# Kernel tuning notes

Measured on AMD Instinct MI355X. Metric: run time of the kernel, lower is better.

The kernel has to match this reference:

```python
import jax, jax.numpy as jnp
import numpy as np

KERNEL_SIZE = 11
OUT_CH = 512
IN_CH = 512


def make_pos_grid(k):
    # centered integer offsets, grid flattened at the end: shape (2, k*k)
    coords = jnp.arange(k, dtype=jnp.float32) - (k - 1) / 2.0
    yy, xx = jnp.meshgrid(coords, coords, indexing="ij")
    return jnp.stack([yy.reshape(-1), xx.reshape(-1)], axis=0)  # (2, k*k)


def setup_inputs() -> dict:
    key = jax.random.key(0)
    k1, _ = jax.random.split(key)
    # raw Cholesky parameters per (out_channel, in_channel) pair; diagonal goes
    # through exp() in reference() to guarantee positive-definite covariances.
    chol_raw = 0.1 * jax.random.normal(k1, (OUT_CH, IN_CH, 2, 2), dtype=jnp.float32)
    pos_grid = make_pos_grid(KERNEL_SIZE)
    return {"chol_raw": chol_raw, "pos_grid": pos_grid}


def reference(chol_raw, pos_grid):
    # chol_raw: (O, I, 2, 2) raw params; pos_grid: (2, K) with K = k*k
    O, I = chol_raw.shape[0], chol_raw.shape[1]
    K = pos_grid.shape[-1]
    k = int(round(np.sqrt(K)))

    # Lower-triangular Cholesky factor with positive diagonal:
    # L = [[exp(a), 0], [c, exp(d)]]
    l11 = jnp.exp(chol_raw[..., 0, 0])[..., None]  # (O, I, 1)
    l21 = chol_raw[..., 1, 0][..., None]           # (O, I, 1)
    l22 = jnp.exp(chol_raw[..., 1, 1])[..., None]  # (O, I, 1)

    x1 = pos_grid[0]  # (K,)
    x2 = pos_grid[1]  # (K,)

    # Inlined forward substitution: solve L b = x for each (o, i, position)
    b1 = x1 / l11                    # (O, I, K)
    b2 = (x2 - l21 * b1) / l22       # (O, I, K)

    # dists = sum over the 2-vector of squares = x^T S^{-1} x
    dists = (b1 * b1 + b2 * b2).reshape((O, I, k, k))
    return dists
```

## Files before the change

kernel.cpp:

```cpp
#include <hip/hip_runtime.h>

#define KK 121
#define NPAIR (512 * 512)
#define PPB 64
#define NBLK (NPAIR / PPB)
#define STAGE_F4 (PPB * KK / 4)

__global__ __launch_bounds__(256) void
quad_rank3_kernel(const float4* __restrict__ chol4,
                  const float* __restrict__ pg,
                  float4* __restrict__ out4) {
    __shared__ float4 s_uvw[KK];
    __shared__ __align__(16) float stage[PPB * KK];

    const int t = threadIdx.x;

    if (t < KK) {
        float x1 = pg[t];
        float x2 = pg[KK + t];
        float4 g;
        g.x = x1 * x1; g.y = x2 * x2; g.z = x1 * x2; g.w = 0.f;
        s_uvw[t] = g;
    }

    const int p       = t & 63;
    const int quarter = t >> 6;
    const int k0 = (quarter == 0) ? 0 : (30 * quarter + 1);
    const int k1 = (quarter == 0) ? 31 : (k0 + 30);

    float4 c = chol4[blockIdx.x * PPB + p];
    float e1 = __expf(-c.x);
    float e2 = __expf(-c.w);
    float f  = c.z * e2;
    float P  = e1 * e1 * fmaf(f, f, 1.f);
    float Q  = e2 * e2;
    float R  = -2.f * f * e1 * e2;

    __syncthreads();

    float* st = &stage[p * KK];
#pragma unroll 5
    for (int k = k0; k < k1; ++k) {
        float4 g = s_uvw[k];
        st[k] = fmaf(P, g.x, fmaf(Q, g.y, R * g.z));
    }

    __syncthreads();

    const float4* s4 = (const float4*)stage;
    float4* o = out4 + (size_t)blockIdx.x * STAGE_F4;
#pragma unroll
    for (int i = t; i < STAGE_F4; i += 256) {
        o[i] = s4[i];
    }
}

extern "C" void kernel_launch(void* const* d_in, const int* in_sizes, int n_in,
                              void* d_out, int out_size, void* d_ws, size_t ws_size,
                              hipStream_t stream) {
    const float4* chol4 = (const float4*)d_in[0];
    const float* pg     = (const float*)d_in[1];
    float4* out4        = (float4*)d_out;

    quad_rank3_kernel<<<NBLK, 256, 0, stream>>>(chol4, pg, out4);
}
```

Baseline: 131.3 us.

## Compute outputs directly per float4 and stream with nontemporal stores, dropping LDS staging

Removes the 31KB shared-memory staging buffer and the second barrier. Each thread now computes four consecutive output elements straight from per-pair coefficients and grid terms held in shared memory, using a multiply-shift division by 121, and writes them with nontemporal float4 stores. Launch bounds now request 8 blocks per CU. The aim is higher occupancy and less LDS traffic in a write-bound kernel, at the cost of extra index arithmetic and scattered LDS reads per element.

```diff
diff --git a/kernel.cpp b/kernel.cpp
--- a/kernel.cpp
+++ b/kernel.cpp
@@ -4,54 +4,51 @@
 #define NPAIR (512 * 512)
 #define PPB 64
 #define NBLK (NPAIR / PPB)
-#define STAGE_F4 (PPB * KK / 4)
+#define F4PB (PPB * KK / 4)
 
-__global__ __launch_bounds__(256) void
-quad_rank3_kernel(const float4* __restrict__ chol4,
-                  const float* __restrict__ pg,
-                  float4* __restrict__ out4) {
+typedef float floatx4 __attribute__((ext_vector_type(4)));
+
+__global__ __launch_bounds__(256, 8) void
+quad_stream_kernel(const float4* __restrict__ chol4,
+                   const float* __restrict__ pg,
+                   float4* __restrict__ out4) {
+    __shared__ float4 s_pqr[PPB];
     __shared__ float4 s_uvw[KK];
-    __shared__ __align__(16) float stage[PPB * KK];
 
     const int t = threadIdx.x;
 
     if (t < KK) {
         float x1 = pg[t];
         float x2 = pg[KK + t];
-        float4 g;
-        g.x = x1 * x1; g.y = x2 * x2; g.z = x1 * x2; g.w = 0.f;
-        s_uvw[t] = g;
+        s_uvw[t] = make_float4(x1 * x1, x2 * x2, x1 * x2, 0.f);
     }
-
-    const int p       = t & 63;
-    const int quarter = t >> 6;
-    const int k0 = (quarter == 0) ? 0 : (30 * quarter + 1);
-    const int k1 = (quarter == 0) ? 31 : (k0 + 30);
-
-    float4 c = chol4[blockIdx.x * PPB + p];
-    float e1 = __expf(-c.x);
-    float e2 = __expf(-c.w);
-    float f  = c.z * e2;
-    float P  = e1 * e1 * fmaf(f, f, 1.f);
-    float Q  = e2 * e2;
-    float R  = -2.f * f * e1 * e2;
-
+    if (t < PPB) {
+        float4 c = chol4[blockIdx.x * PPB + t];
+        float e1 = __expf(-c.x);
+        float e2 = __expf(-c.w);
+        float f  = c.z * e2;
+        float P  = e1 * e1 * fmaf(f, f, 1.f);
+        float Q  = e2 * e2;
+        float R  = -2.f * f * e1 * e2;
+        s_pqr[t] = make_float4(P, Q, R, 0.f);
+    }
     __syncthreads();
 
-    float* st = &stage[p * KK];
-#pragma unroll 5
-    for (int k = k0; k < k1; ++k) {
-        float4 g = s_uvw[k];
-        st[k] = fmaf(P, g.x, fmaf(Q, g.y, R * g.z));
-    }
-
-    __syncthreads();
-
-    const float4* s4 = (const float4*)stage;
-    float4* o = out4 + (size_t)blockIdx.x * STAGE_F4;
+    floatx4* o = (floatx4*)(out4 + (size_t)blockIdx.x * F4PB);
+#pragma unroll 2
+    for (int i = t; i < F4PB; i += 256) {
+        const int f0 = 4 * i;
+        floatx4 res;
 #pragma unroll
-    for (int i = t; i < STAGE_F4; i += 256) {
-        o[i] = s4[i];
+        for (int e = 0; e < 4; ++e) {
+            const int fe = f0 + e;
+            const int p  = (fe * 17333) >> 21;
+            const int k  = fe - 121 * p;
+            const float4 pqr = s_pqr[p];
+            const float4 uvw = s_uvw[k];
+            res[e] = fmaf(pqr.x, uvw.x, fmaf(pqr.y, uvw.y, pqr.z * uvw.z));
+        }
+        __builtin_nontemporal_store(res, &o[i]);
     }
 }
 
@@ -62,5 +59,5 @@
     const float* pg     = (const float*)d_in[1];
     float4* out4        = (float4*)d_out;
 
-    quad_rank3_kernel<<<NBLK, 256, 0, stream>>>(chol4, pg, out4);
+    quad_stream_kernel<<<NBLK, 256, 0, stream>>>(chol4, pg, out4);
 }
```

Result: slower. 152.2 us (+15.9%).
